# Kernel optimization log

Measured on AMD Instinct MI355X. Metric: run time of the kernel, lower is better.

Reference implementation:

```python
import jax, jax.numpy as jnp
import numpy as np

EMBED_DIM = 1024
HEAD_DIM = 128

def setup_inputs() -> dict:
    key = jax.random.key(0)
    ks = jax.random.split(key, 7)
    B, S = 4, 2048
    x = jax.random.normal(ks[0], (B, S, EMBED_DIM), dtype=jnp.float32)
    # Linear params: weight [embed_dim, head_dim] (applied as x @ W + b), scaled init
    scale = 1.0 / np.sqrt(EMBED_DIM)
    Wq = jax.random.normal(ks[1], (EMBED_DIM, HEAD_DIM), dtype=jnp.float32) * scale
    Wk = jax.random.normal(ks[2], (EMBED_DIM, HEAD_DIM), dtype=jnp.float32) * scale
    Wv = jax.random.normal(ks[3], (EMBED_DIM, HEAD_DIM), dtype=jnp.float32) * scale
    bq = jax.random.normal(ks[4], (HEAD_DIM,), dtype=jnp.float32) * 0.01
    bk = jax.random.normal(ks[5], (HEAD_DIM,), dtype=jnp.float32) * 0.01
    bv = jax.random.normal(ks[6], (HEAD_DIM,), dtype=jnp.float32) * 0.01
    return {"x": x, "Wq": Wq, "bq": bq, "Wk": Wk, "bk": bk, "Wv": Wv, "bv": bv}

def reference(x, Wq, bq, Wk, bk, Wv, bv):
    # x: [B, S, E]
    S = x.shape[1]
    norm = jnp.asarray(HEAD_DIM ** 0.5, x.dtype)
    q = x @ Wq + bq  # [B, S, D]
    k = x @ Wk + bk
    v = x @ Wv + bv
    scores = jnp.einsum('bsd,btd->bst', q, k) / norm  # [B, S, S]
    causal = jnp.tril(jnp.ones((S, S), dtype=bool))
    scores = jnp.where(causal, scores, -jnp.inf)
    att = jax.nn.softmax(scores, axis=-1)
    return jnp.einsum('bst,btd->bsd', att, v)  # [B, S, D]
```

## Files before the change

### kernel.cpp

```cpp
#include <hip/hip_runtime.h>
#include <hip/hip_bf16.h>

typedef __attribute__((ext_vector_type(8))) short short8;
typedef __attribute__((ext_vector_type(4))) float f32x4;

static __device__ __forceinline__ unsigned short f2bf(float f){
  union { float f; unsigned int u; } v; v.f = f;
  unsigned int r = v.u + 0x7fffu + ((v.u >> 16) & 1u);
  return (unsigned short)(r >> 16);
}

static __device__ __forceinline__ void load_lds16(const unsigned short* g, unsigned short* l){
  __builtin_amdgcn_global_load_lds(
      (const __attribute__((address_space(1))) unsigned int*)(g),
      (__attribute__((address_space(3))) unsigned int*)(l), 16, 0, 0);
}

__global__ void k_prep(const float* __restrict__ x, unsigned short* __restrict__ xb,
                       const float* __restrict__ Wq, const float* __restrict__ Wk,
                       const float* __restrict__ Wv,
                       const float* __restrict__ bq, const float* __restrict__ bk,
                       const float* __restrict__ bv,
                       unsigned short* __restrict__ Wt, float* __restrict__ bias){
  int bx = blockIdx.x;
  int tid = threadIdx.x;
  if (bx < 4096){
    int i = (bx * 256 + tid) * 8;
    float4 a = *(const float4*)(x + i);
    float4 b = *(const float4*)(x + i + 4);
    unsigned short h[8];
    h[0]=f2bf(a.x); h[1]=f2bf(a.y); h[2]=f2bf(a.z); h[3]=f2bf(a.w);
    h[4]=f2bf(b.x); h[5]=f2bf(b.y); h[6]=f2bf(b.z); h[7]=f2bf(b.w);
    *(uint4*)(xb + i) = *(uint4*)h;
  } else {
    int gid = (bx - 4096) * 256 + tid;
    int p = gid >> 17;
    int rem = gid & 131071;
    int d = rem >> 10, e = rem & 1023;
    const float* W = (p==0) ? Wq : ((p==1) ? Wk : Wv);
    Wt[gid] = f2bf(W[e*128 + d]);
    if (gid < 384){
      int pp = gid >> 7, dd = gid & 127;
      bias[gid] = (pp==0) ? bq[dd] : ((pp==1) ? bk[dd] : bv[dd]);
    }
  }
}

__global__ __launch_bounds__(256) void k_gemm_qkv(
    const unsigned short* __restrict__ Xb, const unsigned short* __restrict__ Wt,
    const float* __restrict__ bias,
    unsigned short* __restrict__ Qsw, unsigned short* __restrict__ Ksw,
    unsigned short* __restrict__ Vsw){
  __shared__ __align__(16) char smem[49152];
  float* Lf = (float*)smem;
  int tid = threadIdx.x;
  int mt = blockIdx.x;
  int p  = blockIdx.y;
  int m0 = mt * 64;
  int w = tid >> 6, lane = tid & 63, quad = lane >> 4, l16 = lane & 15;
  int wm = (w >> 1) * 32, wn = (w & 1) * 64;
  f32x4 acc[2][4];
  #pragma unroll
  for (int i=0;i<2;i++)
    #pragma unroll
    for (int j=0;j<4;j++) acc[i][j] = (f32x4){0.f,0.f,0.f,0.f};

  const unsigned short* Wp = Wt + p * (128*1024);
  const unsigned short* Ag = Xb + (m0 + w*16 + (lane>>3))*1024 + (lane&7)*8;
  const unsigned short* Bg = Wp + (w*32 + (lane>>3))*1024 + (lane&7)*8;
  int aoff = (w*16)*64;
  int boff = (w*32)*64;

  auto stage = [&](int sel, int k0){
    unsigned short* Al = (unsigned short*)(smem + sel*24576) + aoff;
    unsigned short* Bl = (unsigned short*)(smem + sel*24576 + 8192) + boff;
    load_lds16(Ag + k0, Al);
    load_lds16(Ag + k0 + 8192, Al + 512);
    #pragma unroll
    for (int s8=0; s8<4; s8++) load_lds16(Bg + k0 + s8*8192, Bl + s8*512);
  };

  stage(0, 0);
  __syncthreads();
  int cur = 0;
  for (int t=0; t<16; t++){
    if (t < 15) stage(cur^1, (t+1)*64);
    const unsigned short* Ac = (const unsigned short*)(smem + cur*24576);
    const unsigned short* Bc = Ac + 4096;
    #pragma unroll
    for (int kk=0; kk<64; kk+=32){
      short8 af[2], bf[4];
      #pragma unroll
      for (int i=0;i<2;i++) af[i] = *(const short8*)(Ac + (wm + i*16 + l16)*64 + kk + quad*8);
      #pragma unroll
      for (int j=0;j<4;j++) bf[j] = *(const short8*)(Bc + (wn + j*16 + l16)*64 + kk + quad*8);
      #pragma unroll
      for (int i=0;i<2;i++)
        #pragma unroll
        for (int j=0;j<4;j++)
          acc[i][j] = __builtin_amdgcn_mfma_f32_16x16x32_bf16(af[i], bf[j], acc[i][j], 0,0,0);
    }
    __syncthreads();
    cur ^= 1;
  }

  const float qscale = 0.08838834764831845f;
  if (p == 2){
    #pragma unroll
    for (int i=0;i<2;i++)
      #pragma unroll
      for (int j=0;j<4;j++){
        int grow0 = m0 + wm + i*16 + quad*4;
        int col = wn + j*16 + l16;
        unsigned short pk[4];
        float bv_ = bias[256 + col];
        #pragma unroll
        for (int r=0;r<4;r++) pk[r] = f2bf(acc[i][j][r] + bv_);
        int bb2 = grow0 >> 11, s = grow0 & 2047;
        int t64 = s >> 6, srem = s & 63;
        int kc2 = srem >> 5, q2 = (srem >> 3) & 3, jj = srem & 7;
        int nt = col >> 4, l2 = col & 15;
        *(uint2*)(Vsw + (bb2*32+t64)*8192 + nt*1024 + kc2*512 + q2*128 + l2*8 + jj) = *(uint2*)pk;
      }
  } else {
    #pragma unroll
    for (int i=0;i<2;i++)
      #pragma unroll
      for (int j=0;j<4;j++)
        #pragma unroll
        for (int r=0;r<4;r++)
          Lf[(wm + i*16 + quad*4 + r)*128 + wn + j*16 + l16] = acc[i][j][r];
    __syncthreads();
    unsigned short* dst = (p==0)? Qsw : Ksw;
    float scale = (p==0)? qscale : 1.0f;
    #pragma unroll
    for (int it=0; it<8; it++){
      int g = it*256 + tid;
      int row = g >> 5, cs = (g & 31)*4;
      f32x4 a = *(const f32x4*)(Lf + row*128 + cs);
      int grow = m0 + row;
      int rt = grow >> 4, m = grow & 15;
      int kc = cs >> 5, q2 = (cs >> 3) & 3, jj = cs & 7;
      unsigned short pk[4];
      #pragma unroll
      for (int k=0;k<4;k++) pk[k] = f2bf((a[k] + bias[p*128+cs+k])*scale);
      *(uint2*)(dst + rt*2048 + kc*512 + q2*128 + m*8 + jj) = *(uint2*)pk;
    }
  }
}

__global__ __launch_bounds__(256) void k_attn(
    const unsigned short* __restrict__ Qsw, const unsigned short* __restrict__ Ksw,
    const unsigned short* __restrict__ Vsw, float* __restrict__ out){
  __shared__ __align__(16) float Ob[4*2112];
  __shared__ float Ml[4][2][16];
  __shared__ __align__(16) unsigned short Pw[4*1280];
  int x = blockIdx.x;
  int b = x & 3;
  int qb = x >> 2;
  int T64 = (qb >> 2) + 1;
  int tid = threadIdx.x;
  int w = tid >> 6;
  int lane = tid & 63;
  int quad = lane >> 4, l16 = lane & 15;
  int qs = qb * 16;

  short8 aq[4];
  #pragma unroll
  for (int kc=0;kc<4;kc++)
    aq[kc] = *(const short8*)(Qsw + (b*128 + qb)*2048 + kc*512 + lane*8);

  f32x4 o[8];
  #pragma unroll
  for (int i=0;i<8;i++) o[i] = (f32x4){0.f,0.f,0.f,0.f};
  float mcol = -1e30f;
  float lcol = 0.f;
  short8 ap[2];
  unsigned short* Pws = Pw + w*1280;

  const unsigned short* Kb = Ksw + b*128*2048;
  const unsigned short* Vb = Vsw + b*32*8192;

  for (int tt = w; tt < T64; tt += 4){
    int t0 = tt * 64;
    short8 kf[16];
    #pragma unroll
    for (int nt=0;nt<4;nt++){
      const unsigned short* Kt = Kb + ((t0>>4)+nt)*2048 + lane*8;
      #pragma unroll
      for (int kc=0;kc<4;kc++)
        kf[nt*4+kc] = *(const short8*)(Kt + kc*512);
    }
    f32x4 sc[4];
    #pragma unroll
    for (int nt=0;nt<4;nt++) sc[nt] = (f32x4){0.f,0.f,0.f,0.f};
    __builtin_amdgcn_s_setprio(1);
    #pragma unroll
    for (int nt=0;nt<4;nt++)
      #pragma unroll
      for (int kc=0;kc<4;kc++)
        sc[nt] = __builtin_amdgcn_mfma_f32_16x16x32_bf16(kf[nt*4+kc], aq[kc], sc[nt], 0,0,0);
    __builtin_amdgcn_s_setprio(0);
    short8 vf[16];
    const unsigned short* Vt0 = Vb + (t0>>6)*8192 + lane*8;
    #pragma unroll
    for (int nt=0;nt<8;nt++)
      #pragma unroll
      for (int kc2=0;kc2<2;kc2++)
        vf[nt*2+kc2] = *(const short8*)(Vt0 + nt*1024 + kc2*512);

    if (t0 + 63 > qs){
      #pragma unroll
      for (int nt=0;nt<4;nt++){
        int kb_ = t0 + nt*16 + quad*4;
        #pragma unroll
        for (int r=0;r<4;r++)
          if (kb_ + r > qs + l16) sc[nt][r] = -1e30f;
      }
    }
    float mt_ = -1e30f;
    #pragma unroll
    for (int nt=0;nt<4;nt++)
      #pragma unroll
      for (int r=0;r<4;r++) mt_ = fmaxf(mt_, sc[nt][r]);
    mt_ = fmaxf(mt_, __shfl_xor(mt_, 16));
    mt_ = fmaxf(mt_, __shfl_xor(mt_, 32));
    float mn = fmaxf(mcol, mt_);
    float al = __expf(mcol - mn);
    mcol = mn;
    float ls = 0.f;
    #pragma unroll
    for (int nt=0;nt<4;nt++)
      #pragma unroll
      for (int r=0;r<4;r++){
        float pv = __expf(sc[nt][r] - mn);
        sc[nt][r] = pv;
        ls += pv;
      }
    ls += __shfl_xor(ls, 16);
    ls += __shfl_xor(ls, 32);
    lcol = lcol*al + ls;
    #pragma unroll
    for (int r=0;r<4;r++){
      float ar = __shfl(al, quad*4 + r);
      #pragma unroll
      for (int nt=0;nt<8;nt++) o[nt][r] *= ar;
    }
    #pragma unroll
    for (int nt=0;nt<4;nt++){
      unsigned short pk[4];
      #pragma unroll
      for (int r=0;r<4;r++) pk[r] = f2bf(sc[nt][r]);
      *(uint2*)(Pws + l16*80 + nt*16 + quad*4) = *(uint2*)pk;
    }
    ap[0] = *(const short8*)(Pws + l16*80 + quad*8);
    ap[1] = *(const short8*)(Pws + l16*80 + 32 + quad*8);
    __builtin_amdgcn_s_setprio(1);
    #pragma unroll
    for (int nt=0; nt<8; nt++)
      #pragma unroll
      for (int kc2=0;kc2<2;kc2++)
        o[nt] = __builtin_amdgcn_mfma_f32_16x16x32_bf16(ap[kc2], vf[nt*2+kc2], o[nt], 0,0,0);
    __builtin_amdgcn_s_setprio(0);
  }

  #pragma unroll
  for (int nt=0;nt<8;nt++)
    #pragma unroll
    for (int r=0;r<4;r++)
      Ob[w*2112 + (quad*4 + r)*132 + nt*16 + l16] = o[nt][r];
  if (quad == 0){
    Ml[w][0][l16] = mcol;
    Ml[w][1][l16] = lcol;
  }
  __syncthreads();

  int row = tid >> 4;
  int c0 = (tid & 15) * 8;
  float m0_ = fmaxf(fmaxf(Ml[0][0][row], Ml[1][0][row]),
                    fmaxf(Ml[2][0][row], Ml[3][0][row]));
  f32x4 acc0 = (f32x4){0.f,0.f,0.f,0.f};
  f32x4 acc1 = (f32x4){0.f,0.f,0.f,0.f};
  float lsum = 0.f;
  #pragma unroll
  for (int ww=0; ww<4; ww++){
    float e = __expf(Ml[ww][0][row] - m0_);
    lsum += Ml[ww][1][row] * e;
    const float* Or = Ob + ww*2112 + row*132 + c0;
    acc0 += *(const f32x4*)(Or)     * e;
    acc1 += *(const f32x4*)(Or + 4) * e;
  }
  float inv = 1.0f / lsum;
  float* op = out + (size_t)(b*2048 + qs + row)*128 + c0;
  acc0 *= inv; acc1 *= inv;
  *(f32x4*)(op)     = acc0;
  *(f32x4*)(op + 4) = acc1;
}

extern "C" void kernel_launch(void* const* d_in, const int* in_sizes, int n_in,
                              void* d_out, int out_size, void* d_ws, size_t ws_size,
                              hipStream_t stream) {
  const float* x  = (const float*)d_in[0];
  const float* Wq = (const float*)d_in[1];
  const float* bq = (const float*)d_in[2];
  const float* Wk = (const float*)d_in[3];
  const float* bk = (const float*)d_in[4];
  const float* Wv = (const float*)d_in[5];
  const float* bv = (const float*)d_in[6];
  char* ws = (char*)d_ws;
  unsigned short* Xb   = (unsigned short*)(ws);
  unsigned short* Wt   = (unsigned short*)(ws + 16777216);
  float*          bias = (float*)(ws + 17563648);
  unsigned short* Qsw  = (unsigned short*)(ws + 17565184);
  unsigned short* Ksw  = (unsigned short*)(ws + 19662336);
  unsigned short* Vsw  = (unsigned short*)(ws + 21759488);
  float* out = (float*)d_out;

  hipLaunchKernelGGL(k_prep,    dim3(5632),    dim3(256), 0, stream,
                     x, Xb, Wq, Wk, Wv, bq, bk, bv, Wt, bias);
  hipLaunchKernelGGL(k_gemm_qkv,dim3(128,3),   dim3(256), 0, stream,
                     Xb, Wt, bias, Qsw, Ksw, Vsw);
  hipLaunchKernelGGL(k_attn,    dim3(512),     dim3(256), 0, stream,
                     Qsw, Ksw, Vsw, out);
}
```

Before: 123.8 us.

## Fuse fp32-to-bf16 conversion of x into QKV GEMM A-tile loading

The separate pass that converted x to bf16 and wrote it to workspace is removed. The GEMM now loads fp32 x into registers, converts to bf16, and stores into a padded LDS A tile (row stride 72) after the MFMA loop, so the next tile's load is prefetched during compute. The grid is also flattened and remapped so the three projections of an M tile land on the same XCD for L2 reuse of x. The cost is that each x tile is read in fp32 three times (once per projection), and register-staged loads replace direct global-to-LDS copies for A.

```diff
diff --git a/kernel.cpp b/kernel.cpp
--- a/kernel.cpp
+++ b/kernel.cpp
@@ -16,46 +16,37 @@
       (__attribute__((address_space(3))) unsigned int*)(l), 16, 0, 0);
 }
 
-__global__ void k_prep(const float* __restrict__ x, unsigned short* __restrict__ xb,
-                       const float* __restrict__ Wq, const float* __restrict__ Wk,
+__global__ void k_prep(const float* __restrict__ Wq, const float* __restrict__ Wk,
                        const float* __restrict__ Wv,
                        const float* __restrict__ bq, const float* __restrict__ bk,
                        const float* __restrict__ bv,
                        unsigned short* __restrict__ Wt, float* __restrict__ bias){
-  int bx = blockIdx.x;
-  int tid = threadIdx.x;
-  if (bx < 4096){
-    int i = (bx * 256 + tid) * 8;
-    float4 a = *(const float4*)(x + i);
-    float4 b = *(const float4*)(x + i + 4);
-    unsigned short h[8];
-    h[0]=f2bf(a.x); h[1]=f2bf(a.y); h[2]=f2bf(a.z); h[3]=f2bf(a.w);
-    h[4]=f2bf(b.x); h[5]=f2bf(b.y); h[6]=f2bf(b.z); h[7]=f2bf(b.w);
-    *(uint4*)(xb + i) = *(uint4*)h;
-  } else {
-    int gid = (bx - 4096) * 256 + tid;
-    int p = gid >> 17;
-    int rem = gid & 131071;
-    int d = rem >> 10, e = rem & 1023;
-    const float* W = (p==0) ? Wq : ((p==1) ? Wk : Wv);
-    Wt[gid] = f2bf(W[e*128 + d]);
-    if (gid < 384){
-      int pp = gid >> 7, dd = gid & 127;
-      bias[gid] = (pp==0) ? bq[dd] : ((pp==1) ? bk[dd] : bv[dd]);
-    }
+  int gid = blockIdx.x * 256 + threadIdx.x;
+  int p = gid >> 17;
+  int rem = gid & 131071;
+  int d = rem >> 10, e = rem & 1023;
+  const float* W = (p==0) ? Wq : ((p==1) ? Wk : Wv);
+  Wt[gid] = f2bf(W[e*128 + d]);
+  if (gid < 384){
+    int pp = gid >> 7, dd = gid & 127;
+    bias[gid] = (pp==0) ? bq[dd] : ((pp==1) ? bk[dd] : bv[dd]);
   }
 }
 
 __global__ __launch_bounds__(256) void k_gemm_qkv(
-    const unsigned short* __restrict__ Xb, const unsigned short* __restrict__ Wt,
+    const float* __restrict__ x, const unsigned short* __restrict__ Wt,
     const float* __restrict__ bias,
     unsigned short* __restrict__ Qsw, unsigned short* __restrict__ Ksw,
     unsigned short* __restrict__ Vsw){
-  __shared__ __align__(16) char smem[49152];
+  __shared__ __align__(16) char smem[51200];
   float* Lf = (float*)smem;
   int tid = threadIdx.x;
-  int mt = blockIdx.x;
-  int p  = blockIdx.y;
+  int bid = blockIdx.x;
+  int xcd = bid & 7;
+  int slot = bid >> 3;
+  int mtl = slot / 3;
+  int p   = slot - mtl*3;
+  int mt  = xcd*16 + mtl;
   int m0 = mt * 64;
   int w = tid >> 6, lane = tid & 63, quad = lane >> 4, l16 = lane & 15;
   int wm = (w >> 1) * 32, wn = (w & 1) * 64;
@@ -65,33 +56,48 @@
     #pragma unroll
     for (int j=0;j<4;j++) acc[i][j] = (f32x4){0.f,0.f,0.f,0.f};
 
+  int arow = tid >> 2;
+  int acg  = tid & 3;
+  const float* Ax = x + (size_t)(m0 + arow)*1024 + acg*16;
+  float4 av[4];
+
   const unsigned short* Wp = Wt + p * (128*1024);
-  const unsigned short* Ag = Xb + (m0 + w*16 + (lane>>3))*1024 + (lane&7)*8;
   const unsigned short* Bg = Wp + (w*32 + (lane>>3))*1024 + (lane&7)*8;
-  int aoff = (w*16)*64;
   int boff = (w*32)*64;
 
-  auto stage = [&](int sel, int k0){
-    unsigned short* Al = (unsigned short*)(smem + sel*24576) + aoff;
-    unsigned short* Bl = (unsigned short*)(smem + sel*24576 + 8192) + boff;
-    load_lds16(Ag + k0, Al);
-    load_lds16(Ag + k0 + 8192, Al + 512);
+  auto aload = [&](int k0){
+    #pragma unroll
+    for (int i=0;i<4;i++) av[i] = *(const float4*)(Ax + k0 + i*4);
+  };
+  auto astore = [&](int sel){
+    unsigned short h[16];
+    #pragma unroll
+    for (int i=0;i<4;i++){
+      h[i*4+0]=f2bf(av[i].x); h[i*4+1]=f2bf(av[i].y);
+      h[i*4+2]=f2bf(av[i].z); h[i*4+3]=f2bf(av[i].w);
+    }
+    unsigned short* Ad = (unsigned short*)(smem + sel*25600) + arow*72 + acg*16;
+    *(uint4*)(Ad)   = *(uint4*)(h);
+    *(uint4*)(Ad+8) = *(uint4*)(h+8);
+  };
+  auto bstage = [&](int sel, int k0){
+    unsigned short* Bl = (unsigned short*)(smem + sel*25600 + 9216) + boff;
     #pragma unroll
     for (int s8=0; s8<4; s8++) load_lds16(Bg + k0 + s8*8192, Bl + s8*512);
   };
 
-  stage(0, 0);
+  aload(0); bstage(0, 0); astore(0);
   __syncthreads();
   int cur = 0;
   for (int t=0; t<16; t++){
-    if (t < 15) stage(cur^1, (t+1)*64);
-    const unsigned short* Ac = (const unsigned short*)(smem + cur*24576);
-    const unsigned short* Bc = Ac + 4096;
+    if (t < 15){ aload((t+1)*64); bstage(cur^1, (t+1)*64); }
+    const unsigned short* Ac = (const unsigned short*)(smem + cur*25600);
+    const unsigned short* Bc = Ac + 4608;
     #pragma unroll
     for (int kk=0; kk<64; kk+=32){
       short8 af[2], bf[4];
       #pragma unroll
-      for (int i=0;i<2;i++) af[i] = *(const short8*)(Ac + (wm + i*16 + l16)*64 + kk + quad*8);
+      for (int i=0;i<2;i++) af[i] = *(const short8*)(Ac + (wm + i*16 + l16)*72 + kk + quad*8);
       #pragma unroll
       for (int j=0;j<4;j++) bf[j] = *(const short8*)(Bc + (wn + j*16 + l16)*64 + kk + quad*8);
       #pragma unroll
@@ -100,6 +106,7 @@
         for (int j=0;j<4;j++)
           acc[i][j] = __builtin_amdgcn_mfma_f32_16x16x32_bf16(af[i], bf[j], acc[i][j], 0,0,0);
     }
+    if (t < 15) astore(cur^1);
     __syncthreads();
     cur ^= 1;
   }
@@ -308,18 +315,17 @@
   const float* Wv = (const float*)d_in[5];
   const float* bv = (const float*)d_in[6];
   char* ws = (char*)d_ws;
-  unsigned short* Xb   = (unsigned short*)(ws);
-  unsigned short* Wt   = (unsigned short*)(ws + 16777216);
-  float*          bias = (float*)(ws + 17563648);
-  unsigned short* Qsw  = (unsigned short*)(ws + 17565184);
-  unsigned short* Ksw  = (unsigned short*)(ws + 19662336);
-  unsigned short* Vsw  = (unsigned short*)(ws + 21759488);
+  unsigned short* Wt   = (unsigned short*)(ws);
+  float*          bias = (float*)(ws + 786432);
+  unsigned short* Qsw  = (unsigned short*)(ws + 788480);
+  unsigned short* Ksw  = (unsigned short*)(ws + 2885632);
+  unsigned short* Vsw  = (unsigned short*)(ws + 4982784);
   float* out = (float*)d_out;
 
-  hipLaunchKernelGGL(k_prep,    dim3(5632),    dim3(256), 0, stream,
-                     x, Xb, Wq, Wk, Wv, bq, bk, bv, Wt, bias);
-  hipLaunchKernelGGL(k_gemm_qkv,dim3(128,3),   dim3(256), 0, stream,
-                     Xb, Wt, bias, Qsw, Ksw, Vsw);
+  hipLaunchKernelGGL(k_prep,    dim3(1536),    dim3(256), 0, stream,
+                     Wq, Wk, Wv, bq, bk, bv, Wt, bias);
+  hipLaunchKernelGGL(k_gemm_qkv,dim3(384),     dim3(256), 0, stream,
+                     x, Wt, bias, Qsw, Ksw, Vsw);
   hipLaunchKernelGGL(k_attn,    dim3(512),     dim3(256), 0, stream,
                      Qsw, Ksw, Vsw, out);
 }
```

Result: no change. 125.9 us (+1.7%).
